# Kernel tuning notes

Measured on AMD Instinct MI355X. Metric: run time of the kernel, lower is better.

Reference implementation:

```python
import jax, jax.numpy as jnp
import numpy as np

D = 256   # input / vocab dim (hardcoded in module)
H = 256   # hidden_dim
B, M, N = 64, 32, 32
LN_EPS = 1e-6


def setup_inputs() -> dict:
    key = jax.random.key(0)
    ks = jax.random.split(key, 8)
    Hin = D + 2 * H  # column_stack([x_bd, h_i_jm1, h_im1_j])
    inp = {
        "x": jax.random.normal(ks[0], (B, M, N, D), dtype=jnp.float32),
        "W_gate": jax.random.normal(ks[1], (Hin, 5 * H), dtype=jnp.float32) * (1.0 / np.sqrt(Hin)),
        "b_gate": jnp.zeros((5 * H,), dtype=jnp.float32),
        "ln_scale": jnp.ones((H,), dtype=jnp.float32),
        "ln_bias": jnp.zeros((H,), dtype=jnp.float32),
        "W_head": jax.random.normal(ks[2], (H, D), dtype=jnp.float32) * (1.0 / np.sqrt(H)),
        "b_head": jnp.zeros((D,), dtype=jnp.float32),
        "h_init": jax.random.normal(ks[3], (H, 1), dtype=jnp.float32) * 0.05,
    }
    return inp


def _layernorm(x, scale, bias):
    mu = jnp.mean(x, axis=-1, keepdims=True)
    var = jnp.mean(jnp.square(x - mu), axis=-1, keepdims=True)
    return (x - mu) * jax.lax.rsqrt(var + LN_EPS) * scale + bias


def reference(x, W_gate, b_gate, ln_scale, ln_bias, W_head, b_head, h_init):
    b, m, n, d = x.shape
    h = h_init.shape[0]
    h0_bh = jnp.broadcast_to(h_init[:, 0][None, :], (b, h))  # left-edge init per row
    c0_bh = jnp.zeros((b, h), dtype=x.dtype)

    def col_step(carry, xs):
        h_l, c_l = carry                 # left neighbor (b,h)
        x_bd, h_u, c_u = xs              # input pixel, up-neighbor h/c
        xin = jnp.concatenate([x_bd, h_l, h_u], axis=-1)   # (b, d+2h)
        g = xin @ W_gate + b_gate                           # (b, 5h)
        f_c, f_r, i_g, o_g, g_g = jnp.split(g, 5, axis=-1)
        cell = (jax.nn.sigmoid(f_c) * c_l
                + jax.nn.sigmoid(f_r) * c_u
                + jax.nn.sigmoid(i_g) * jnp.tanh(g_g))      # (b,h)
        h_new = jax.nn.sigmoid(o_g) * jnp.tanh(_layernorm(cell, ln_scale, ln_bias))
        logits = h_new @ W_head + b_head                    # (b,d)
        return (h_new, cell), (h_new, cell, logits)

    def row_step(prev_row, x_row):
        prev_h, prev_c = prev_row        # (n,b,h) from row above
        _, (hs, cs, logits) = jax.lax.scan(col_step, (h0_bh, c0_bh), (x_row, prev_h, prev_c))
        return (hs, cs), logits          # logits: (n,b,d)

    x_mnbd = jnp.transpose(x, (1, 2, 0, 3))                 # (m,n,b,d)
    prev_h0 = jnp.broadcast_to(h_init[:, 0][None, None, :], (n, b, h)).astype(x.dtype)
    prev_c0 = jnp.zeros((n, b, h), dtype=x.dtype)
    _, logits_mnbd = jax.lax.scan(row_step, (prev_h0, prev_c0), x_mnbd)
    return jnp.transpose(logits_mnbd, (2, 0, 1, 3))         # (b,m,n,d)
```

## Files before the change

kernel.cpp:

```cpp
#include <hip/hip_runtime.h>

constexpr int kB   = 64;
constexpr int kM   = 32;
constexpr int kN   = 32;
constexpr int kD   = 256;
constexpr int kH   = 256;
constexpr int kG5  = 1280;

typedef __attribute__((ext_vector_type(8)))  short bf16x8;
typedef __attribute__((ext_vector_type(16))) float f32x16;

__device__ __forceinline__ float bu2f(unsigned short u) {
    return __uint_as_float(((unsigned)u) << 16);
}
__device__ __forceinline__ unsigned short f2bu(float f) {
    unsigned u = __float_as_uint(f);
    return (unsigned short)((u + 0x7FFF + ((u >> 16) & 1)) >> 16);
}
__device__ __forceinline__ void split1(float a, unsigned short& hi, unsigned short& lo) {
    hi = f2bu(a);
    lo = f2bu(a - bu2f(hi));
}
__device__ __forceinline__ float sigm(float x) { return 1.f / (1.f + expf(-x)); }

__global__ void prep_w(const float* __restrict__ Wg,
                       unsigned short* __restrict__ whi,
                       unsigned short* __restrict__ wlo) {
    const int t = blockIdx.x * 256 + threadIdx.x;
    const int lane = t & 63;
    const int rest = t >> 6;
    const int s = rest % 48;
    const int ntile = rest / 48;
    const int n = ntile * 32 + (lane & 31);
    const int kb = s * 16 + (lane >> 5) * 8;
    unsigned short h8[8], l8[8];
    #pragma unroll
    for (int j = 0; j < 8; ++j) {
        const float a = Wg[(size_t)(kb + j) * kG5 + n];
        split1(a, h8[j], l8[j]);
    }
    *(bf16x8*)(whi + (size_t)t * 8) = *(const bf16x8*)h8;
    *(bf16x8*)(wlo + (size_t)t * 8) = *(const bf16x8*)l8;
}

__global__ void prep_wh(const float* __restrict__ Wh,
                        unsigned short* __restrict__ whh,
                        unsigned short* __restrict__ whl) {
    const int t = blockIdx.x * 256 + threadIdx.x;
    const int lane = t & 63;
    const int rest = t >> 6;
    const int kc = rest & 15;
    const int nt = rest >> 4;
    const int n = nt * 32 + (lane & 31);
    const int kb = kc * 16 + (lane >> 5) * 8;
    unsigned short h8[8], l8[8];
    #pragma unroll
    for (int j = 0; j < 8; ++j) {
        const float a = Wh[(size_t)(kb + j) * kD + n];
        split1(a, h8[j], l8[j]);
    }
    *(bf16x8*)(whh + (size_t)t * 8) = *(const bf16x8*)h8;
    *(bf16x8*)(whl + (size_t)t * 8) = *(const bf16x8*)l8;
}

__global__ void prep_h0f(const float* __restrict__ hinit,
                         unsigned short* __restrict__ h0fh,
                         unsigned short* __restrict__ h0fl) {
    const int idx = blockIdx.x * 256 + threadIdx.x;
    const int lane = idx & 63;
    const int kh = idx >> 6;
    const int k0 = kh * 16 + (lane >> 5) * 8;
    unsigned short h8[8], l8[8];
    #pragma unroll
    for (int j = 0; j < 8; ++j) split1(hinit[k0 + j], h8[j], l8[j]);
    *(bf16x8*)(h0fh + (size_t)idx * 8) = *(const bf16x8*)h8;
    *(bf16x8*)(h0fl + (size_t)idx * 8) = *(const bf16x8*)l8;
}

__global__ void prep_x(const float* __restrict__ x,
                       unsigned short* __restrict__ xfh,
                       unsigned short* __restrict__ xfl) {
    const int t = blockIdx.x * 256 + threadIdx.x;
    const int kq   = t & 31;
    const int b    = (t >> 5) & 63;
    const int cell = t >> 11;
    const float* src = x + (((size_t)b * 1024 + cell) * kD + kq * 8);
    unsigned short h8[8], l8[8];
    #pragma unroll
    for (int j = 0; j < 8; ++j) split1(src[j], h8[j], l8[j]);
    const int mt = b >> 5, kh = kq >> 1;
    const int l  = (b & 31) + 32 * (kq & 1);
    const size_t dst = ((((size_t)cell * 2 + mt) * 16 + kh) * 64 + l) * 8;
    *(bf16x8*)(xfh + dst) = *(const bf16x8*)h8;
    *(bf16x8*)(xfl + dst) = *(const bf16x8*)l8;
}

__global__ __launch_bounds__(256)
void gate_mfma_fast(int d,
                    const unsigned short* __restrict__ xfh,
                    const unsigned short* __restrict__ xfl,
                    const unsigned short* __restrict__ whi,
                    const unsigned short* __restrict__ wlo,
                    const unsigned short* __restrict__ hfh,
                    const unsigned short* __restrict__ hfl,
                    const unsigned short* __restrict__ h0fh,
                    const unsigned short* __restrict__ h0fl,
                    float* __restrict__ gates) {
    const int tid = threadIdx.x;
    const int ilo = max(0, d - (kN - 1));
    const int cell = blockIdx.x / 20;
    const int nc   = blockIdx.x % 20;
    const int i = ilo + cell;
    const int j = d - i;
    const int w = tid >> 6, lane = tid & 63;
    const int ln31 = lane & 31, ln5 = lane >> 5;
    const int mt = w & 1;
    const int ntile = nc * 2 + (w >> 1);
    const int hp = (d + 1) & 1;
    const int cl = i * kN + j;

    f32x16 acc;
    #pragma unroll
    for (int r = 0; r < 16; ++r) acc[r] = 0.f;

    const unsigned short* wph = whi + ((size_t)ntile * 3072 + lane) * 8;
    const unsigned short* wpl = wlo + ((size_t)ntile * 3072 + lane) * 8;

    const unsigned short* xph = xfh + (((size_t)cl * 2 + mt) * 16 * 64 + lane) * 8;
    const unsigned short* xpl = xfl + (((size_t)cl * 2 + mt) * 16 * 64 + lane) * 8;
    #pragma unroll 4
    for (int kh = 0; kh < 16; ++kh) {
        const bf16x8 ah = *(const bf16x8*)(xph + (size_t)kh * 512);
        const bf16x8 al = *(const bf16x8*)(xpl + (size_t)kh * 512);
        const bf16x8 wh = *(const bf16x8*)(wph + (size_t)kh * 512);
        const bf16x8 wl = *(const bf16x8*)(wpl + (size_t)kh * 512);
        acc = __builtin_amdgcn_mfma_f32_32x32x16_bf16(ah, wh, acc, 0, 0, 0);
        acc = __builtin_amdgcn_mfma_f32_32x32x16_bf16(ah, wl, acc, 0, 0, 0);
        acc = __builtin_amdgcn_mfma_f32_32x32x16_bf16(al, wh, acc, 0, 0, 0);
    }

    const unsigned short *plh, *pll, *puh, *pul;
    if (j > 0) {
        const size_t o = ((size_t)(hp * kM + i)) * 16384 + ((size_t)(mt * 16) * 64 + lane) * 8;
        plh = hfh + o; pll = hfl + o;
    } else {
        plh = h0fh + lane * 8; pll = h0fl + lane * 8;
    }
    if (i > 0) {
        const size_t o = ((size_t)(hp * kM + (i - 1))) * 16384 + ((size_t)(mt * 16) * 64 + lane) * 8;
        puh = hfh + o; pul = hfl + o;
    } else {
        puh = h0fh + lane * 8; pul = h0fl + lane * 8;
    }

    #pragma unroll 4
    for (int kh = 0; kh < 16; ++kh) {
        const bf16x8 ah = *(const bf16x8*)(plh + (size_t)kh * 512);
        const bf16x8 al = *(const bf16x8*)(pll + (size_t)kh * 512);
        const bf16x8 wh = *(const bf16x8*)(wph + (size_t)(16 + kh) * 512);
        const bf16x8 wl = *(const bf16x8*)(wpl + (size_t)(16 + kh) * 512);
        acc = __builtin_amdgcn_mfma_f32_32x32x16_bf16(ah, wh, acc, 0, 0, 0);
        acc = __builtin_amdgcn_mfma_f32_32x32x16_bf16(ah, wl, acc, 0, 0, 0);
        acc = __builtin_amdgcn_mfma_f32_32x32x16_bf16(al, wh, acc, 0, 0, 0);
    }
    #pragma unroll 4
    for (int kh = 0; kh < 16; ++kh) {
        const bf16x8 ah = *(const bf16x8*)(puh + (size_t)kh * 512);
        const bf16x8 al = *(const bf16x8*)(pul + (size_t)kh * 512);
        const bf16x8 wh = *(const bf16x8*)(wph + (size_t)(32 + kh) * 512);
        const bf16x8 wl = *(const bf16x8*)(wpl + (size_t)(32 + kh) * 512);
        acc = __builtin_amdgcn_mfma_f32_32x32x16_bf16(ah, wh, acc, 0, 0, 0);
        acc = __builtin_amdgcn_mfma_f32_32x32x16_bf16(ah, wl, acc, 0, 0, 0);
        acc = __builtin_amdgcn_mfma_f32_32x32x16_bf16(al, wh, acc, 0, 0, 0);
    }

    const int col = ntile * 32 + ln31;
    #pragma unroll
    for (int r = 0; r < 16; ++r) {
        const int mrow = (r & 3) + 8 * (r >> 2) + 4 * ln5;
        const int bb = mt * 32 + mrow;
        gates[((size_t)i * kB + bb) * kG5 + col] = acc[r];
    }
}

__global__ __launch_bounds__(256)
void gate_mfma_legacy(int d,
               const float* __restrict__ x,
               const unsigned short* __restrict__ whi,
               const unsigned short* __restrict__ wlo,
               const unsigned short* __restrict__ hfh,
               const unsigned short* __restrict__ hfl,
               const unsigned short* __restrict__ h0fh,
               const unsigned short* __restrict__ h0fl,
               float* __restrict__ gates) {
    const int tid = threadIdx.x;
    const int ilo = max(0, d - (kN - 1));
    const int cell = blockIdx.x / 20;
    const int nc   = blockIdx.x % 20;
    const int i = ilo + cell;
    const int j = d - i;
    const int w = tid >> 6, lane = tid & 63;
    const int ln31 = lane & 31, ln5 = lane >> 5;
    const int mt = w & 1;
    const int ntile = nc * 2 + (w >> 1);
    const int hp = (d + 1) & 1;

    f32x16 acc;
    #pragma unroll
    for (int r = 0; r < 16; ++r) acc[r] = 0.f;

    const unsigned short* wph = whi + ((size_t)ntile * 3072 + lane) * 8;
    const unsigned short* wpl = wlo + ((size_t)ntile * 3072 + lane) * 8;

    const int b = mt * 32 + ln31;
    const float* xr = x + (((size_t)b * kM + i) * kN + j) * kD + ln5 * 8;
    #pragma unroll 4
    for (int kh = 0; kh < 16; ++kh) {
        const float4 v0 = *(const float4*)(xr + kh * 16);
        const float4 v1 = *(const float4*)(xr + kh * 16 + 4);
        unsigned short h8[8], l8[8];
        split1(v0.x, h8[0], l8[0]); split1(v0.y, h8[1], l8[1]);
        split1(v0.z, h8[2], l8[2]); split1(v0.w, h8[3], l8[3]);
        split1(v1.x, h8[4], l8[4]); split1(v1.y, h8[5], l8[5]);
        split1(v1.z, h8[6], l8[6]); split1(v1.w, h8[7], l8[7]);
        const bf16x8 ah = *(const bf16x8*)h8;
        const bf16x8 al = *(const bf16x8*)l8;
        const bf16x8 wh = *(const bf16x8*)(wph + (size_t)kh * 512);
        const bf16x8 wl = *(const bf16x8*)(wpl + (size_t)kh * 512);
        acc = __builtin_amdgcn_mfma_f32_32x32x16_bf16(ah, wh, acc, 0, 0, 0);
        acc = __builtin_amdgcn_mfma_f32_32x32x16_bf16(ah, wl, acc, 0, 0, 0);
        acc = __builtin_amdgcn_mfma_f32_32x32x16_bf16(al, wh, acc, 0, 0, 0);
    }

    const unsigned short *plh, *pll, *puh, *pul;
    if (j > 0) {
        const size_t o = ((size_t)(hp * kM + i)) * 16384 + ((size_t)(mt * 16) * 64 + lane) * 8;
        plh = hfh + o; pll = hfl + o;
    } else {
        plh = h0fh + lane * 8; pll = h0fl + lane * 8;
    }
    if (i > 0) {
        const size_t o = ((size_t)(hp * kM + (i - 1))) * 16384 + ((size_t)(mt * 16) * 64 + lane) * 8;
        puh = hfh + o; pul = hfl + o;
    } else {
        puh = h0fh + lane * 8; pul = h0fl + lane * 8;
    }

    #pragma unroll 4
    for (int kh = 0; kh < 16; ++kh) {
        const bf16x8 ah = *(const bf16x8*)(plh + (size_t)kh * 512);
        const bf16x8 al = *(const bf16x8*)(pll + (size_t)kh * 512);
        const bf16x8 wh = *(const bf16x8*)(wph + (size_t)(16 + kh) * 512);
        const bf16x8 wl = *(const bf16x8*)(wpl + (size_t)(16 + kh) * 512);
        acc = __builtin_amdgcn_mfma_f32_32x32x16_bf16(ah, wh, acc, 0, 0, 0);
        acc = __builtin_amdgcn_mfma_f32_32x32x16_bf16(ah, wl, acc, 0, 0, 0);
        acc = __builtin_amdgcn_mfma_f32_32x32x16_bf16(al, wh, acc, 0, 0, 0);
    }
    #pragma unroll 4
    for (int kh = 0; kh < 16; ++kh) {
        const bf16x8 ah = *(const bf16x8*)(puh + (size_t)kh * 512);
        const bf16x8 al = *(const bf16x8*)(pul + (size_t)kh * 512);
        const bf16x8 wh = *(const bf16x8*)(wph + (size_t)(32 + kh) * 512);
        const bf16x8 wl = *(const bf16x8*)(wpl + (size_t)(32 + kh) * 512);
        acc = __builtin_amdgcn_mfma_f32_32x32x16_bf16(ah, wh, acc, 0, 0, 0);
        acc = __builtin_amdgcn_mfma_f32_32x32x16_bf16(ah, wl, acc, 0, 0, 0);
        acc = __builtin_amdgcn_mfma_f32_32x32x16_bf16(al, wh, acc, 0, 0, 0);
    }

    const int col = ntile * 32 + ln31;
    #pragma unroll
    for (int r = 0; r < 16; ++r) {
        const int mrow = (r & 3) + 8 * (r >> 2) + 4 * ln5;
        const int bb = mt * 32 + mrow;
        gates[((size_t)i * kB + bb) * kG5 + col] = acc[r];
    }
}

__global__ __launch_bounds__(256)
void cell_ln(int d,
             const float* __restrict__ bg,
             const float* __restrict__ lns,
             const float* __restrict__ lnb,
             const float* __restrict__ gates,
             float* __restrict__ c_bufs,
             unsigned short* __restrict__ hfh,
             unsigned short* __restrict__ hfl,
             float* out) {
    __shared__ float red[8];
    const int tid = threadIdx.x;
    const int ilo = max(0, d - (kN - 1));
    const int i = ilo + (blockIdx.x >> 4);
    const int j = d - i;
    const int b0 = (blockIdx.x & 15) * 4;
    const int plane = kM * kB * kH;
    const float* c_prev = c_bufs + ((d + 1) & 1) * plane;
    float*       c_cur  = c_bufs + (d & 1) * plane;
    const int hp = d & 1;
    unsigned* outp = (unsigned*)out;

    const int u = tid;
    const float bg0 = bg[u];
    const float bg1 = bg[kH + u];
    const float bg2 = bg[2 * kH + u];
    const float bg3 = bg[3 * kH + u];
    const float bg4 = bg[4 * kH + u];
    const float lnsc = lns[u];
    const float lnbi = lnb[u];
    const int lane = tid & 63, wid = tid >> 6;
    const int kh = u >> 4, r = u & 15, jj = r & 7;

    for (int bl = 0; bl < 4; ++bl) {
        const int b = b0 + bl;
        const float* grow = gates + ((size_t)i * kB + b) * kG5;
        const float fc = grow[u] + bg0;
        const float fr = grow[kH + u] + bg1;
        const float ig = grow[2 * kH + u] + bg2;
        const float og = grow[3 * kH + u] + bg3;
        const float gg = grow[4 * kH + u] + bg4;
        const float cl = (j > 0) ? c_prev[((size_t)i * kB + b) * kH + u] : 0.f;
        const float cu = (i > 0) ? c_prev[((size_t)(i - 1) * kB + b) * kH + u] : 0.f;

        const float cell_v = sigm(fc) * cl + sigm(fr) * cu + sigm(ig) * tanhf(gg);
        c_cur[((size_t)i * kB + b) * kH + u] = cell_v;

        float s = cell_v, s2 = cell_v * cell_v;
        #pragma unroll
        for (int off = 32; off; off >>= 1) {
            s  += __shfl_down(s,  off, 64);
            s2 += __shfl_down(s2, off, 64);
        }
        if (lane == 0) { red[wid] = s; red[4 + wid] = s2; }
        __syncthreads();
        const float sum = red[0] + red[1] + red[2] + red[3];
        const float sq  = red[4] + red[5] + red[6] + red[7];
        __syncthreads();

        const float mu   = sum * (1.f / kH);
        const float var  = sq * (1.f / kH) - mu * mu;
        const float rstd = rsqrtf(var + 1e-6f);
        const float hv   = sigm(og) * tanhf((cell_v - mu) * rstd * lnsc + lnbi);

        unsigned short hb, lb;
        split1(hv, hb, lb);
        const int mt2 = b >> 5;
        const int fl = (b & 31) + 32 * (r >> 3);
        const size_t fo = ((size_t)(hp * kM + i)) * 16384
                        + (((size_t)(mt2 * 16 + kh) * 64 + fl) * 8 + jj);
        hfh[fo] = hb; hfl[fo] = lb;
        outp[(((size_t)b * kM + i) * kN + j) * kD + u] = (unsigned)hb | ((unsigned)lb << 16);
    }
}

__global__ __launch_bounds__(256)
void head_mfma(const unsigned short* __restrict__ whh,
               const unsigned short* __restrict__ whl,
               const float* __restrict__ bh,
               float* out) {
    const int tid = threadIdx.x;
    const int lane = tid & 63, w = tid >> 6;
    const int ln31 = lane & 31, ln5 = lane >> 5;
    const int r0 = blockIdx.x * 64;
    const int mt = w & 1, ng = w >> 1;
    unsigned* outp = (unsigned*)out;

    f32x16 acc[4];
    #pragma unroll
    for (int t = 0; t < 4; ++t)
        #pragma unroll
        for (int r = 0; r < 16; ++r) acc[t][r] = 0.f;

    const int m = r0 + mt * 32 + ln31;
    const unsigned* arow = outp + (size_t)m * kD + ln5 * 8;

    #pragma unroll 2
    for (int kc = 0; kc < 16; ++kc) {
        const uint4 p0 = *(const uint4*)(arow + kc * 16);
        const uint4 p1 = *(const uint4*)(arow + kc * 16 + 4);
        unsigned short h8[8], l8[8];
        h8[0] = (unsigned short)(p0.x & 0xffffu); l8[0] = (unsigned short)(p0.x >> 16);
        h8[1] = (unsigned short)(p0.y & 0xffffu); l8[1] = (unsigned short)(p0.y >> 16);
        h8[2] = (unsigned short)(p0.z & 0xffffu); l8[2] = (unsigned short)(p0.z >> 16);
        h8[3] = (unsigned short)(p0.w & 0xffffu); l8[3] = (unsigned short)(p0.w >> 16);
        h8[4] = (unsigned short)(p1.x & 0xffffu); l8[4] = (unsigned short)(p1.x >> 16);
        h8[5] = (unsigned short)(p1.y & 0xffffu); l8[5] = (unsigned short)(p1.y >> 16);
        h8[6] = (unsigned short)(p1.z & 0xffffu); l8[6] = (unsigned short)(p1.z >> 16);
        h8[7] = (unsigned short)(p1.w & 0xffffu); l8[7] = (unsigned short)(p1.w >> 16);
        const bf16x8 ah = *(const bf16x8*)h8;
        const bf16x8 al = *(const bf16x8*)l8;
        #pragma unroll
        for (int t = 0; t < 4; ++t) {
            const int nt = ng * 4 + t;
            const size_t g = ((size_t)(nt * 16 + kc) * 64 + lane) * 8;
            const bf16x8 wh = *(const bf16x8*)(whh + g);
            const bf16x8 wl = *(const bf16x8*)(whl + g);
            acc[t] = __builtin_amdgcn_mfma_f32_32x32x16_bf16(ah, wh, acc[t], 0, 0, 0);
            acc[t] = __builtin_amdgcn_mfma_f32_32x32x16_bf16(ah, wl, acc[t], 0, 0, 0);
            acc[t] = __builtin_amdgcn_mfma_f32_32x32x16_bf16(al, wh, acc[t], 0, 0, 0);
        }
    }

    __syncthreads();

    #pragma unroll
    for (int t = 0; t < 4; ++t) {
        const int col = (ng * 4 + t) * 32 + ln31;
        const float bb = bh[col];
        #pragma unroll
        for (int r = 0; r < 16; ++r) {
            const int row = r0 + mt * 32 + (r & 3) + 8 * (r >> 2) + 4 * ln5;
            out[(size_t)row * kD + col] = acc[t][r] + bb;
        }
    }
}

extern "C" void kernel_launch(void* const* d_in, const int* in_sizes, int n_in,
                              void* d_out, int out_size, void* d_ws, size_t ws_size,
                              hipStream_t stream) {
    const float* x     = (const float*)d_in[0];
    const float* Wg    = (const float*)d_in[1];
    const float* bg    = (const float*)d_in[2];
    const float* lns   = (const float*)d_in[3];
    const float* lnb   = (const float*)d_in[4];
    const float* Wh    = (const float*)d_in[5];
    const float* bh    = (const float*)d_in[6];
    const float* hinit = (const float*)d_in[7];
    float* out = (float*)d_out;

    char* wsb = (char*)d_ws;
    float*          gates  = (float*)(wsb);
    float*          c_bufs = (float*)(wsb + 10485760);
    unsigned short* hfh    = (unsigned short*)(wsb + 14680064);
    unsigned short* hfl    = (unsigned short*)(wsb + 16777216);
    unsigned short* whi    = (unsigned short*)(wsb + 18874368);
    unsigned short* wlo    = (unsigned short*)(wsb + 20840448);
    unsigned short* h0fh   = (unsigned short*)(wsb + 22806528);
    unsigned short* h0fl   = (unsigned short*)(wsb + 22822912);
    unsigned short* whh    = (unsigned short*)(wsb + 22839296);
    unsigned short* whl    = (unsigned short*)(wsb + 22970368);
    unsigned short* xfh    = (unsigned short*)(wsb + 23101440);
    unsigned short* xfl    = (unsigned short*)(wsb + 56655872);
    const size_t kWsNeededFast = 90210304;

    const bool fast = (ws_size >= kWsNeededFast);

    hipLaunchKernelGGL(prep_w,  dim3(480), dim3(256), 0, stream, Wg, whi, wlo);
    hipLaunchKernelGGL(prep_wh, dim3(32),  dim3(256), 0, stream, Wh, whh, whl);
    hipLaunchKernelGGL(prep_h0f, dim3(4),  dim3(256), 0, stream, hinit, h0fh, h0fl);
    if (fast)
        hipLaunchKernelGGL(prep_x, dim3(8192), dim3(256), 0, stream, x, xfh, xfl);

    for (int d = 0; d < kM + kN - 1; ++d) {
        const int ilo = max(0, d - (kN - 1));
        const int ihi = min(d, kM - 1);
        const int ncell = ihi - ilo + 1;
        if (fast) {
            hipLaunchKernelGGL(gate_mfma_fast, dim3(ncell * 20), dim3(256), 0, stream,
                               d, xfh, xfl, whi, wlo, hfh, hfl, h0fh, h0fl, gates);
        } else {
            hipLaunchKernelGGL(gate_mfma_legacy, dim3(ncell * 20), dim3(256), 0, stream,
                               d, x, whi, wlo, hfh, hfl, h0fh, h0fl, gates);
        }
        hipLaunchKernelGGL(cell_ln, dim3(ncell * 16), dim3(256), 0, stream,
                           d, bg, lns, lnb, gates, c_bufs, hfh, hfl, out);
    }
    hipLaunchKernelGGL(head_mfma, dim3(1024), dim3(256), 0, stream, whh, whl, bh, out);
}
```

Baseline: 1.876 ms.

## Fuse gate GEMM and cell/LayerNorm per diagonal using per-cell atomic barriers

Merges the per-diagonal gate MFMA kernel and the cell/LayerNorm kernel into one launch. The 20 blocks of each cell sync through an atomic counter (release/acquire spin), and then 16 of them run the cell update. This halves the kernel launches and inter-kernel gaps along the 63-step wavefront. The spin-wait depends on all 20 blocks of a cell being co-resident (deadlock risk), and it adds a counter array to the workspace that prep_h0f zeroes.

```diff
diff --git a/kernel.cpp b/kernel.cpp
--- a/kernel.cpp
+++ b/kernel.cpp
@@ -65,16 +65,20 @@
 
 __global__ void prep_h0f(const float* __restrict__ hinit,
                          unsigned short* __restrict__ h0fh,
-                         unsigned short* __restrict__ h0fl) {
+                         unsigned short* __restrict__ h0fl,
+                         unsigned* __restrict__ cnt) {
     const int idx = blockIdx.x * 256 + threadIdx.x;
-    const int lane = idx & 63;
-    const int kh = idx >> 6;
-    const int k0 = kh * 16 + (lane >> 5) * 8;
-    unsigned short h8[8], l8[8];
-    #pragma unroll
-    for (int j = 0; j < 8; ++j) split1(hinit[k0 + j], h8[j], l8[j]);
-    *(bf16x8*)(h0fh + (size_t)idx * 8) = *(const bf16x8*)h8;
-    *(bf16x8*)(h0fl + (size_t)idx * 8) = *(const bf16x8*)l8;
+    if (idx < 1024) {
+        const int lane = idx & 63;
+        const int kh = idx >> 6;
+        const int k0 = kh * 16 + (lane >> 5) * 8;
+        unsigned short h8[8], l8[8];
+        #pragma unroll
+        for (int j = 0; j < 8; ++j) split1(hinit[k0 + j], h8[j], l8[j]);
+        *(bf16x8*)(h0fh + (size_t)idx * 8) = *(const bf16x8*)h8;
+        *(bf16x8*)(h0fl + (size_t)idx * 8) = *(const bf16x8*)l8;
+    }
+    if (idx < 63 * 32) cnt[idx] = 0;
 }
 
 __global__ void prep_x(const float* __restrict__ x,
@@ -95,8 +99,8 @@
     *(bf16x8*)(xfl + dst) = *(const bf16x8*)l8;
 }
 
-__global__ __launch_bounds__(256)
-void gate_mfma_fast(int d,
+__device__ __forceinline__
+void gate_unit_body(int d, int unit,
                     const unsigned short* __restrict__ xfh,
                     const unsigned short* __restrict__ xfl,
                     const unsigned short* __restrict__ whi,
@@ -108,8 +112,8 @@
                     float* __restrict__ gates) {
     const int tid = threadIdx.x;
     const int ilo = max(0, d - (kN - 1));
-    const int cell = blockIdx.x / 20;
-    const int nc   = blockIdx.x % 20;
+    const int cell = unit / 20;
+    const int nc   = unit % 20;
     const int i = ilo + cell;
     const int j = d - i;
     const int w = tid >> 6, lane = tid & 63;
@@ -181,6 +185,116 @@
         const int bb = mt * 32 + mrow;
         gates[((size_t)i * kB + bb) * kG5 + col] = acc[r];
     }
+}
+
+__device__ __forceinline__
+void cell_unit_body(int d, int unit,
+                    const float* __restrict__ bg,
+                    const float* __restrict__ lns,
+                    const float* __restrict__ lnb,
+                    const float* __restrict__ gates,
+                    float* __restrict__ c_bufs,
+                    unsigned short* __restrict__ hfh,
+                    unsigned short* __restrict__ hfl,
+                    float* out) {
+    __shared__ float red[8];
+    const int tid = threadIdx.x;
+    const int ilo = max(0, d - (kN - 1));
+    const int i = ilo + (unit >> 4);
+    const int j = d - i;
+    const int b0 = (unit & 15) * 4;
+    const int plane = kM * kB * kH;
+    const float* c_prev = c_bufs + ((d + 1) & 1) * plane;
+    float*       c_cur  = c_bufs + (d & 1) * plane;
+    const int hp = d & 1;
+    unsigned* outp = (unsigned*)out;
+
+    const int u = tid;
+    const float bg0 = bg[u];
+    const float bg1 = bg[kH + u];
+    const float bg2 = bg[2 * kH + u];
+    const float bg3 = bg[3 * kH + u];
+    const float bg4 = bg[4 * kH + u];
+    const float lnsc = lns[u];
+    const float lnbi = lnb[u];
+    const int lane = tid & 63, wid = tid >> 6;
+    const int kh = u >> 4, r = u & 15, jj = r & 7;
+
+    for (int bl = 0; bl < 4; ++bl) {
+        const int b = b0 + bl;
+        const float* grow = gates + ((size_t)i * kB + b) * kG5;
+        const float fc = grow[u] + bg0;
+        const float fr = grow[kH + u] + bg1;
+        const float ig = grow[2 * kH + u] + bg2;
+        const float og = grow[3 * kH + u] + bg3;
+        const float gg = grow[4 * kH + u] + bg4;
+        const float cl = (j > 0) ? c_prev[((size_t)i * kB + b) * kH + u] : 0.f;
+        const float cu = (i > 0) ? c_prev[((size_t)(i - 1) * kB + b) * kH + u] : 0.f;
+
+        const float cell_v = sigm(fc) * cl + sigm(fr) * cu + sigm(ig) * tanhf(gg);
+        c_cur[((size_t)i * kB + b) * kH + u] = cell_v;
+
+        float s = cell_v, s2 = cell_v * cell_v;
+        #pragma unroll
+        for (int off = 32; off; off >>= 1) {
+            s  += __shfl_down(s,  off, 64);
+            s2 += __shfl_down(s2, off, 64);
+        }
+        if (lane == 0) { red[wid] = s; red[4 + wid] = s2; }
+        __syncthreads();
+        const float sum = red[0] + red[1] + red[2] + red[3];
+        const float sq  = red[4] + red[5] + red[6] + red[7];
+        __syncthreads();
+
+        const float mu   = sum * (1.f / kH);
+        const float var  = sq * (1.f / kH) - mu * mu;
+        const float rstd = rsqrtf(var + 1e-6f);
+        const float hv   = sigm(og) * tanhf((cell_v - mu) * rstd * lnsc + lnbi);
+
+        unsigned short hb, lb;
+        split1(hv, hb, lb);
+        const int mt2 = b >> 5;
+        const int fl = (b & 31) + 32 * (r >> 3);
+        const size_t fo = ((size_t)(hp * kM + i)) * 16384
+                        + (((size_t)(mt2 * 16 + kh) * 64 + fl) * 8 + jj);
+        hfh[fo] = hb; hfl[fo] = lb;
+        outp[(((size_t)b * kM + i) * kN + j) * kD + u] = (unsigned)hb | ((unsigned)lb << 16);
+    }
+}
+
+__global__ __launch_bounds__(256, 4)
+void gate_cell(int d,
+               const unsigned short* __restrict__ xfh,
+               const unsigned short* __restrict__ xfl,
+               const unsigned short* __restrict__ whi,
+               const unsigned short* __restrict__ wlo,
+               unsigned short* __restrict__ hfh,
+               unsigned short* __restrict__ hfl,
+               const unsigned short* __restrict__ h0fh,
+               const unsigned short* __restrict__ h0fl,
+               float* __restrict__ gates,
+               const float* __restrict__ bg,
+               const float* __restrict__ lns,
+               const float* __restrict__ lnb,
+               float* __restrict__ c_bufs,
+               float* out,
+               unsigned* __restrict__ cnt) {
+    const int cell = blockIdx.x / 20;
+    const int nc   = blockIdx.x % 20;
+
+    gate_unit_body(d, blockIdx.x, xfh, xfl, whi, wlo, hfh, hfl, h0fh, h0fl, gates);
+
+    __threadfence();
+    __syncthreads();
+    unsigned* c = cnt + d * 32 + cell;
+    if (threadIdx.x == 0) {
+        __hip_atomic_fetch_add(c, 1u, __ATOMIC_RELEASE, __HIP_MEMORY_SCOPE_AGENT);
+        while (__hip_atomic_load(c, __ATOMIC_ACQUIRE, __HIP_MEMORY_SCOPE_AGENT) < 20u) {}
+    }
+    __syncthreads();
+
+    if (nc < 16)
+        cell_unit_body(d, cell * 16 + nc, bg, lns, lnb, gates, c_bufs, hfh, hfl, out);
 }
 
 __global__ __launch_bounds__(256)
@@ -286,69 +400,7 @@
              unsigned short* __restrict__ hfh,
              unsigned short* __restrict__ hfl,
              float* out) {
-    __shared__ float red[8];
-    const int tid = threadIdx.x;
-    const int ilo = max(0, d - (kN - 1));
-    const int i = ilo + (blockIdx.x >> 4);
-    const int j = d - i;
-    const int b0 = (blockIdx.x & 15) * 4;
-    const int plane = kM * kB * kH;
-    const float* c_prev = c_bufs + ((d + 1) & 1) * plane;
-    float*       c_cur  = c_bufs + (d & 1) * plane;
-    const int hp = d & 1;
-    unsigned* outp = (unsigned*)out;
-
-    const int u = tid;
-    const float bg0 = bg[u];
-    const float bg1 = bg[kH + u];
-    const float bg2 = bg[2 * kH + u];
-    const float bg3 = bg[3 * kH + u];
-    const float bg4 = bg[4 * kH + u];
-    const float lnsc = lns[u];
-    const float lnbi = lnb[u];
-    const int lane = tid & 63, wid = tid >> 6;
-    const int kh = u >> 4, r = u & 15, jj = r & 7;
-
-    for (int bl = 0; bl < 4; ++bl) {
-        const int b = b0 + bl;
-        const float* grow = gates + ((size_t)i * kB + b) * kG5;
-        const float fc = grow[u] + bg0;
-        const float fr = grow[kH + u] + bg1;
-        const float ig = grow[2 * kH + u] + bg2;
-        const float og = grow[3 * kH + u] + bg3;
-        const float gg = grow[4 * kH + u] + bg4;
-        const float cl = (j > 0) ? c_prev[((size_t)i * kB + b) * kH + u] : 0.f;
-        const float cu = (i > 0) ? c_prev[((size_t)(i - 1) * kB + b) * kH + u] : 0.f;
-
-        const float cell_v = sigm(fc) * cl + sigm(fr) * cu + sigm(ig) * tanhf(gg);
-        c_cur[((size_t)i * kB + b) * kH + u] = cell_v;
-
-        float s = cell_v, s2 = cell_v * cell_v;
-        #pragma unroll
-        for (int off = 32; off; off >>= 1) {
-            s  += __shfl_down(s,  off, 64);
-            s2 += __shfl_down(s2, off, 64);
-        }
-        if (lane == 0) { red[wid] = s; red[4 + wid] = s2; }
-        __syncthreads();
-        const float sum = red[0] + red[1] + red[2] + red[3];
-        const float sq  = red[4] + red[5] + red[6] + red[7];
-        __syncthreads();
-
-        const float mu   = sum * (1.f / kH);
-        const float var  = sq * (1.f / kH) - mu * mu;
-        const float rstd = rsqrtf(var + 1e-6f);
-        const float hv   = sigm(og) * tanhf((cell_v - mu) * rstd * lnsc + lnbi);
-
-        unsigned short hb, lb;
-        split1(hv, hb, lb);
-        const int mt2 = b >> 5;
-        const int fl = (b & 31) + 32 * (r >> 3);
-        const size_t fo = ((size_t)(hp * kM + i)) * 16384
-                        + (((size_t)(mt2 * 16 + kh) * 64 + fl) * 8 + jj);
-        hfh[fo] = hb; hfl[fo] = lb;
-        outp[(((size_t)b * kM + i) * kN + j) * kD + u] = (unsigned)hb | ((unsigned)lb << 16);
-    }
+    cell_unit_body(d, blockIdx.x, bg, lns, lnb, gates, c_bufs, hfh, hfl, out);
 }
 
 __global__ __launch_bounds__(256)
@@ -437,31 +489,37 @@
     unsigned short* h0fl   = (unsigned short*)(wsb + 22822912);
     unsigned short* whh    = (unsigned short*)(wsb + 22839296);
     unsigned short* whl    = (unsigned short*)(wsb + 22970368);
-    unsigned short* xfh    = (unsigned short*)(wsb + 23101440);
-    unsigned short* xfl    = (unsigned short*)(wsb + 56655872);
-    const size_t kWsNeededFast = 90210304;
+    unsigned*       cnt    = (unsigned*)(wsb + 23101440);
+    unsigned short* xfh    = (unsigned short*)(wsb + 23111680);
+    unsigned short* xfl    = (unsigned short*)(wsb + 56666112);
+    const size_t kWsNeededFast = 90220544;
 
     const bool fast = (ws_size >= kWsNeededFast);
 
     hipLaunchKernelGGL(prep_w,  dim3(480), dim3(256), 0, stream, Wg, whi, wlo);
     hipLaunchKernelGGL(prep_wh, dim3(32),  dim3(256), 0, stream, Wh, whh, whl);
-    hipLaunchKernelGGL(prep_h0f, dim3(4),  dim3(256), 0, stream, hinit, h0fh, h0fl);
-    if (fast)
+    hipLaunchKernelGGL(prep_h0f, dim3(8),  dim3(256), 0, stream, hinit, h0fh, h0fl, cnt);
+
+    if (fast) {
         hipLaunchKernelGGL(prep_x, dim3(8192), dim3(256), 0, stream, x, xfh, xfl);
-
-    for (int d = 0; d < kM + kN - 1; ++d) {
-        const int ilo = max(0, d - (kN - 1));
-        const int ihi = min(d, kM - 1);
-        const int ncell = ihi - ilo + 1;
-        if (fast) {
-            hipLaunchKernelGGL(gate_mfma_fast, dim3(ncell * 20), dim3(256), 0, stream,
-                               d, xfh, xfl, whi, wlo, hfh, hfl, h0fh, h0fl, gates);
-        } else {
+        for (int d = 0; d < kM + kN - 1; ++d) {
+            const int ilo = max(0, d - (kN - 1));
+            const int ihi = min(d, kM - 1);
+            const int ncell = ihi - ilo + 1;
+            hipLaunchKernelGGL(gate_cell, dim3(ncell * 20), dim3(256), 0, stream,
+                               d, xfh, xfl, whi, wlo, hfh, hfl, h0fh, h0fl,
+                               gates, bg, lns, lnb, c_bufs, out, cnt);
+        }
+    } else {
+        for (int d = 0; d < kM + kN - 1; ++d) {
+            const int ilo = max(0, d - (kN - 1));
+            const int ihi = min(d, kM - 1);
+            const int ncell = ihi - ilo + 1;
             hipLaunchKernelGGL(gate_mfma_legacy, dim3(ncell * 20), dim3(256), 0, stream,
                                d, x, whi, wlo, hfh, hfl, h0fh, h0fl, gates);
+            hipLaunchKernelGGL(cell_ln, dim3(ncell * 16), dim3(256), 0, stream,
+                               d, bg, lns, lnb, gates, c_bufs, hfh, hfl, out);
         }
-        hipLaunchKernelGGL(cell_ln, dim3(ncell * 16), dim3(256), 0, stream,
-                           d, bg, lns, lnb, gates, c_bufs, hfh, hfl, out);
     }
     hipLaunchKernelGGL(head_mfma, dim3(1024), dim3(256), 0, stream, whh, whl, bh, out);
 }
```

New measurement: 5.479 ms. +192.0%, slower.
